# Performance work log

Measured on AMD Instinct MI355X. Metric: run time of the kernel, lower is better.

The kernel has to match this reference:

```python
import jax, jax.numpy as jnp
import numpy as np

FS = 11        # filter_size
N_ITER = 5     # mean-field iterations


def _unfold(x, fs):
    """x: (B, C, Hp, Wp) padded -> patches (B, C, H, W, fs, fs) with
    patches[b,c,h,w,i,j] == x[b,c,h+i,w+j]."""
    B, C, Hp, Wp = x.shape
    H, W = Hp - fs + 1, Wp - fs + 1
    p = jax.lax.conv_general_dilated_patches(
        x.reshape(B * C, 1, Hp, Wp), (fs, fs), (1, 1), 'VALID')  # (B*C, fs*fs, H, W)
    return p.reshape(B, C, fs, fs, H, W).transpose(0, 1, 4, 5, 2, 3)


def _smoothing_filter(fs, inv_bw, spacings):
    """Gaussian spatial filter with zeroed center, shape (B, fs, fs)."""
    r = jnp.arange(-(fs // 2), fs // 2 + 1, dtype=spacings.dtype)
    d = jnp.stack(jnp.meshgrid(r, r, indexing='ij'))           # (2, fs, fs)
    d = d[None] * spacings[:, :, None, None]                   # (B, 2, fs, fs)
    f = jnp.exp(-jnp.sum((d * inv_bw) ** 2 / 2, axis=1))       # (B, fs, fs)
    return f.at[:, fs // 2, fs // 2].set(0.0)


def setup_inputs() -> dict:
    key = jax.random.key(0)
    k1, k2 = jax.random.split(key)
    B, C, CH, H, W = 2, 6, 3, 192, 192
    return {
        'x': jax.random.normal(k1, (B, C, H, W), dtype=jnp.float32),
        'features': jax.random.normal(k2, (B, CH, H, W), dtype=jnp.float32),
        'spatial_spacings': jnp.ones((B, 2), dtype=jnp.float32),
        'smoothing_weight': jnp.array(1.0, dtype=jnp.float32),
        'appearance_weight': jnp.array(1.0, dtype=jnp.float32),
        'inverse_smoothing_bandwidth': jnp.array(1.0, dtype=jnp.float32),
        'inverse_appearance_bandwidth': jnp.array(1.0, dtype=jnp.float32),
    }


def reference(x, features, spatial_spacings, smoothing_weight, appearance_weight,
              inverse_smoothing_bandwidth, inverse_appearance_bandwidth):
    fs, pad = FS, FS // 2
    B, C, H, W = x.shape
    pad_cfg = [(0, 0), (0, 0), (pad, pad), (pad, pad)]

    # Spatial Gaussian filter (iteration-independent).
    sf = _smoothing_filter(fs, inverse_smoothing_bandwidth, spatial_spacings)  # (B,fs,fs)

    # Bilateral (appearance) filter, also iteration-independent -> hoisted.
    fpatch = _unfold(jnp.pad(features, pad_cfg), fs)           # (B,ch,H,W,fs,fs)
    diffs = features[..., None, None] - fpatch
    af = jnp.exp(-jnp.sum((diffs * inverse_appearance_bandwidth) ** 2 / 2, axis=1))  # (B,H,W,fs,fs)
    af = af.at[..., fs // 2, fs // 2].set(0.0)

    # combined message filter: w_s * sf + w_a * sf * af  (center tap already zero)
    sfb = sf[:, None, None]                                    # (B,1,1,fs,fs)
    total_filter = smoothing_weight * jnp.broadcast_to(sfb, af.shape) + appearance_weight * sfb * af

    compat = -jnp.eye(C, dtype=x.dtype)                        # Potts compatibility mu(l,l') = -[l==l']
    negative_unary = x
    for _ in range(N_ITER):
        q = jax.nn.softmax(x, axis=1)
        qpatch = _unfold(jnp.pad(q, pad_cfg), fs)              # (B,C,H,W,fs,fs)
        msg = jnp.einsum('bhwij,bchwij->bchw', total_filter, qpatch)
        x = negative_unary - jnp.einsum('bjhw,jk->bkhw', msg, compat)
    return jax.nn.log_softmax(x, axis=1)
```

## Files before the change

### kernel.cpp

```cpp
#include <hip/hip_runtime.h>

#define HH 192
#define WW 192
#define BB 2
#define NC 6
#define FSZ 11
#define PAD 5
#define TW 16
#define TH 8
#define SWD 26
#define SHT 18
#define LA 27
#define HW (HH*WW)
#define NWV 12
#define BT (NWV*64)
#define NPX (TW*TH)

__device__ __forceinline__ unsigned pkbf(float a, float b) {
    unsigned ua = (__float_as_uint(a) + 0x8000u) >> 16;
    unsigned ub = (__float_as_uint(b) + 0x8000u) & 0xffff0000u;
    return ua | ub;
}
__device__ __forceinline__ float lo16(unsigned u){ return __uint_as_float(u << 16); }
__device__ __forceinline__ float hi16(unsigned u){ return __uint_as_float(u & 0xffff0000u); }

template<bool FIRST, bool LAST>
__global__ __launch_bounds__(BT, 6)
void crf_it(const float* __restrict__ xpl, const uint4* __restrict__ Ain,
            const float* __restrict__ f2in, const float* __restrict__ feats,
            const float* __restrict__ spac, const float* __restrict__ swp,
            const float* __restrict__ awp, const float* __restrict__ isbp,
            const float* __restrict__ iabp,
            uint4* __restrict__ Aout, float* __restrict__ f2out,
            float* __restrict__ outp)
{
    __shared__ uint4 A[SHT][LA];
    __shared__ float F2[SHT][LA];
    __shared__ float sfw[FSZ*FSZ];
    __shared__ float sfa[FSZ*FSZ];
    __shared__ float pm[NWV][NC][132];

    const int tid = threadIdx.x;
    const int b  = blockIdx.z;
    const int w0 = blockIdx.x * TW;
    const int h0 = blockIdx.y * TH;

    const float sw  = swp[0], aw = awp[0], isb = isbp[0], iab = iabp[0];
    const float s0  = spac[b*2], s1 = spac[b*2+1];
    const float sfac = iab * 0.70710678f;

    if (tid < FSZ*FSZ) {
        const int fi = tid / FSZ, fj = tid - (tid/FSZ)*FSZ;
        const float ri = (float)(fi-PAD) * s0 * isb;
        const float rj = (float)(fj-PAD) * s1 * isb;
        float sf = __expf(-0.5f*(ri*ri + rj*rj));
        if (fi == PAD && fj == PAD) sf = 0.f;
        sfw[tid] = sf * sw;
        sfa[tid] = sf * aw;
    }

    if (tid < SHT*SWD) {
        const int sr = tid / SWD, sc = tid - (tid/SWD)*SWD;
        const int gh = h0 + sr - PAD, gw = w0 + sc - PAD;
        uint4 av = make_uint4(0u,0u,0u,0u);
        float f2v = 0.f;
        if (gh >= 0 && gh < HH && gw >= 0 && gw < WW) {
            if (FIRST) {
                const int off = gh*WW + gw;
                const float* xb = xpl + (size_t)b*NC*HW + off;
                const float v0 = xb[0], v1 = xb[HW], v2 = xb[2*HW];
                const float v3 = xb[3*HW], v4 = xb[4*HW], v5 = xb[5*HW];
                float m = fmaxf(fmaxf(fmaxf(v0,v1),fmaxf(v2,v3)),fmaxf(v4,v5));
                float q0=__expf(v0-m), q1=__expf(v1-m), q2=__expf(v2-m);
                float q3=__expf(v3-m), q4=__expf(v4-m), q5=__expf(v5-m);
                const float rs = 1.0f/(q0+q1+q2+q3+q4+q5);
                const float* fb = feats + (size_t)b*3*HW + off;
                const float g0 = fb[0]*sfac, g1 = fb[HW]*sfac;
                f2v = fb[2*HW]*sfac;
                av = make_uint4(pkbf(q0*rs,q1*rs), pkbf(q2*rs,q3*rs),
                                pkbf(q4*rs,q5*rs), pkbf(g0,g1));
            } else {
                const size_t p = (size_t)(b*HH + gh)*WW + gw;
                av  = Ain[p];
                f2v = f2in[p];
            }
        }
        A[sr][sc]  = av;
        F2[sr][sc] = f2v;
    }
    __syncthreads();

    const int w    = tid >> 6;
    const int l    = tid & 63;
    const int half = l >> 5;
    const int lh   = l & 31;
    const int ry   = lh >> 2;
    const int c0   = (lh & 3) * 4;

    int row, jbase, jcnt;
    if (w == 5)       { row = 5; jbase = half ? 6 : 0; jcnt = 3; }
    else if (w == 11) { row = 5; jbase = half ? 9 : 3; jcnt = half ? 2 : 3; }
    else              { row = w; jbase = half ? 6 : 0; jcnt = half ? 5 : 6; }
    const int asteps = jcnt + 3;

    float srwR[6], sraR[6];
    #pragma unroll
    for (int d = 0; d < 6; ++d) {
        const int j = jbase + d;
        const bool v = (d < jcnt) && (j < FSZ);
        srwR[d] = v ? sfw[row*FSZ + j] : 0.f;
        sraR[d] = v ? sfa[row*FSZ + j] : 0.f;
    }

    float cf0[4], cf1[4], cf2[4];
    #pragma unroll
    for (int k = 0; k < 4; ++k) {
        const unsigned fw = A[ry+PAD][c0+PAD+k].w;
        cf0[k] = lo16(fw);
        cf1[k] = hi16(fw);
        cf2[k] = F2[ry+PAD][c0+PAD+k];
    }

    float2 m01[4], m23[4], m45[4];
    #pragma unroll
    for (int k = 0; k < 4; ++k) {
        m01[k]=make_float2(0.f,0.f); m23[k]=make_float2(0.f,0.f); m45[k]=make_float2(0.f,0.f);
    }

    const uint4* Ar = &A[ry + row][c0 + jbase];
    const float* Fr = &F2[ry + row][c0 + jbase];
    #pragma unroll
    for (int a = 0; a < 9; ++a) {
        if (a < asteps) {
            const uint4 av = Ar[a];
            const float g2 = Fr[a];
            const float q0 = lo16(av.x), q1 = hi16(av.x);
            const float q2 = lo16(av.y), q3 = hi16(av.y);
            const float q4 = lo16(av.z), q5 = hi16(av.z);
            const float g0 = lo16(av.w), g1 = hi16(av.w);
            #pragma unroll
            for (int k = 0; k < 4; ++k) {
                const int d = a - k;
                if (0 <= d && d < 6) {
                    const float d0 = cf0[k]-g0, d1 = cf1[k]-g1, d2 = cf2[k]-g2;
                    const float t  = fmaf(d2,d2, fmaf(d1,d1, d0*d0));
                    const float af = __expf(-t);
                    const float tf = fmaf(af, sraR[d], srwR[d]);
                    m01[k].x = fmaf(tf,q0,m01[k].x); m01[k].y = fmaf(tf,q1,m01[k].y);
                    m23[k].x = fmaf(tf,q2,m23[k].x); m23[k].y = fmaf(tf,q3,m23[k].y);
                    m45[k].x = fmaf(tf,q4,m45[k].x); m45[k].y = fmaf(tf,q5,m45[k].y);
                }
            }
        }
    }

    #pragma unroll
    for (int k = 0; k < 4; ++k) {
        m01[k].x += __shfl_xor(m01[k].x, 32); m01[k].y += __shfl_xor(m01[k].y, 32);
        m23[k].x += __shfl_xor(m23[k].x, 32); m23[k].y += __shfl_xor(m23[k].y, 32);
        m45[k].x += __shfl_xor(m45[k].x, 32); m45[k].y += __shfl_xor(m45[k].y, 32);
    }

    if (half == 0) {
        const int px = ry*16 + c0;
        *(float4*)&pm[w][0][px] = make_float4(m01[0].x, m01[1].x, m01[2].x, m01[3].x);
        *(float4*)&pm[w][1][px] = make_float4(m01[0].y, m01[1].y, m01[2].y, m01[3].y);
        *(float4*)&pm[w][2][px] = make_float4(m23[0].x, m23[1].x, m23[2].x, m23[3].x);
        *(float4*)&pm[w][3][px] = make_float4(m23[0].y, m23[1].y, m23[2].y, m23[3].y);
        *(float4*)&pm[w][4][px] = make_float4(m45[0].x, m45[1].x, m45[2].x, m45[3].x);
        *(float4*)&pm[w][5][px] = make_float4(m45[0].y, m45[1].y, m45[2].y, m45[3].y);
    }
    __syncthreads();

    if (tid < NPX) {
        const int pr = tid >> 4, pc = tid & 15;
        const int oh = h0 + pr, ow = w0 + pc;
        const size_t pb = (size_t)b*NC*HW + (size_t)oh*WW + ow;
        float xn[NC];
        #pragma unroll
        for (int c = 0; c < NC; ++c) {
            float s = 0.f;
            #pragma unroll
            for (int g = 0; g < NWV; ++g) s += pm[g][c][tid];
            xn[c] = s + xpl[pb + (size_t)c*HW];
        }

        float m = xn[0];
        #pragma unroll
        for (int c = 1; c < NC; ++c) m = fmaxf(m, xn[c]);

        if (LAST) {
            float s = 0.f;
            #pragma unroll
            for (int c = 0; c < NC; ++c) s += __expf(xn[c]-m);
            const float lg = m + __logf(s);
            #pragma unroll
            for (int c = 0; c < NC; ++c) outp[pb + (size_t)c*HW] = xn[c] - lg;
        } else {
            float e[NC], s = 0.f;
            #pragma unroll
            for (int c = 0; c < NC; ++c) { e[c] = __expf(xn[c]-m); s += e[c]; }
            const float rs = 1.0f / s;
            const int r5 = pr + PAD, c5 = pc + PAD;
            const size_t p = (size_t)(b*HH + oh)*WW + ow;
            Aout[p] = make_uint4(pkbf(e[0]*rs,e[1]*rs), pkbf(e[2]*rs,e[3]*rs),
                                 pkbf(e[4]*rs,e[5]*rs), A[r5][c5].w);
            if (FIRST) f2out[p] = F2[r5][c5];
        }
    }
}

extern "C" void kernel_launch(void* const* d_in, const int* in_sizes, int n_in,
                              void* d_out, int out_size, void* d_ws, size_t ws_size,
                              hipStream_t stream)
{
    const float* x    = (const float*)d_in[0];
    const float* fts  = (const float*)d_in[1];
    const float* spc  = (const float*)d_in[2];
    const float* swp  = (const float*)d_in[3];
    const float* awp  = (const float*)d_in[4];
    const float* isbp = (const float*)d_in[5];
    const float* iabp = (const float*)d_in[6];
    float* out = (float*)d_out;

    uint4* A0  = (uint4*)d_ws;
    uint4* A1  = A0 + (size_t)BB*HW;
    float* f2s = (float*)(A1 + (size_t)BB*HW);

    dim3 grid(WW/TW, HH/TH, BB);
    dim3 blk(BT);

    crf_it<true ,false><<<grid, blk, 0, stream>>>(x, A1, f2s, fts, spc, swp, awp, isbp, iabp, A0, f2s, out);
    crf_it<false,false><<<grid, blk, 0, stream>>>(x, A0, f2s, fts, spc, swp, awp, isbp, iabp, A1, f2s, out);
    crf_it<false,false><<<grid, blk, 0, stream>>>(x, A1, f2s, fts, spc, swp, awp, isbp, iabp, A0, f2s, out);
    crf_it<false,false><<<grid, blk, 0, stream>>>(x, A0, f2s, fts, spc, swp, awp, isbp, iabp, A1, f2s, out);
    crf_it<false,true ><<<grid, blk, 0, stream>>>(x, A1, f2s, fts, spc, swp, awp, isbp, iabp, A0, f2s, out);
}
```

Before: 63.01 us.

## Retile CRF iteration to 96x3 tiles with shuffle-only tap reduction

Changes the tile from 16x8 to 96x3 pixels per block, so the halo overhead is smaller relative to the tile. Each group of 8 lanes now handles 3 adjacent pixels and splits the 11x11 taps across lanes. The partial sums are combined with xor shuffles, which replaces the shared-memory partial-message buffer and the second barrier. The trade-off is a higher register count per thread (18 accumulators) and fewer blocks per CU (launch bounds drop from 6 to 3). The halo load is now a strided loop.

```diff
diff --git a/kernel.cpp b/kernel.cpp
--- a/kernel.cpp
+++ b/kernel.cpp
@@ -6,15 +6,13 @@
 #define NC 6
 #define FSZ 11
 #define PAD 5
-#define TW 16
-#define TH 8
-#define SWD 26
-#define SHT 18
-#define LA 27
+#define TW 96
+#define TH 3
+#define SWD 107
+#define SHT 14
+#define LA 107
 #define HW (HH*WW)
-#define NWV 12
-#define BT (NWV*64)
-#define NPX (TW*TH)
+#define BT 768
 
 __device__ __forceinline__ unsigned pkbf(float a, float b) {
     unsigned ua = (__float_as_uint(a) + 0x8000u) >> 16;
@@ -25,7 +23,7 @@
 __device__ __forceinline__ float hi16(unsigned u){ return __uint_as_float(u & 0xffff0000u); }
 
 template<bool FIRST, bool LAST>
-__global__ __launch_bounds__(BT, 6)
+__global__ __launch_bounds__(BT, 3)
 void crf_it(const float* __restrict__ xpl, const uint4* __restrict__ Ain,
             const float* __restrict__ f2in, const float* __restrict__ feats,
             const float* __restrict__ spac, const float* __restrict__ swp,
@@ -38,7 +36,6 @@
     __shared__ float F2[SHT][LA];
     __shared__ float sfw[FSZ*FSZ];
     __shared__ float sfa[FSZ*FSZ];
-    __shared__ float pm[NWV][NC][132];
 
     const int tid = threadIdx.x;
     const int b  = blockIdx.z;
@@ -59,8 +56,8 @@
         sfa[tid] = sf * aw;
     }
 
-    if (tid < SHT*SWD) {
-        const int sr = tid / SWD, sc = tid - (tid/SWD)*SWD;
+    for (int idx = tid; idx < SHT*SWD; idx += BT) {
+        const int sr = idx / SWD, sc = idx - (idx/SWD)*SWD;
         const int gh = h0 + sr - PAD, gw = w0 + sc - PAD;
         uint4 av = make_uint4(0u,0u,0u,0u);
         float f2v = 0.f;
@@ -92,46 +89,44 @@
 
     const int w    = tid >> 6;
     const int l    = tid & 63;
-    const int half = l >> 5;
-    const int lh   = l & 31;
-    const int ry   = lh >> 2;
-    const int c0   = (lh & 3) * 4;
-
-    int row, jbase, jcnt;
-    if (w == 5)       { row = 5; jbase = half ? 6 : 0; jcnt = 3; }
-    else if (w == 11) { row = 5; jbase = half ? 9 : 3; jcnt = half ? 2 : 3; }
-    else              { row = w; jbase = half ? 6 : 0; jcnt = half ? 5 : 6; }
-    const int asteps = jcnt + 3;
-
-    float srwR[6], sraR[6];
-    #pragma unroll
-    for (int d = 0; d < 6; ++d) {
-        const int j = jbase + d;
-        const bool v = (d < jcnt) && (j < FSZ);
-        srwR[d] = v ? sfw[row*FSZ + j] : 0.f;
-        sraR[d] = v ? sfa[row*FSZ + j] : 0.f;
-    }
-
-    float cf0[4], cf1[4], cf2[4];
-    #pragma unroll
-    for (int k = 0; k < 4; ++k) {
-        const unsigned fw = A[ry+PAD][c0+PAD+k].w;
-        cf0[k] = lo16(fw);
-        cf1[k] = hi16(fw);
-        cf2[k] = F2[ry+PAD][c0+PAD+k];
-    }
-
-    float2 m01[4], m23[4], m45[4];
-    #pragma unroll
-    for (int k = 0; k < 4; ++k) {
-        m01[k]=make_float2(0.f,0.f); m23[k]=make_float2(0.f,0.f); m45[k]=make_float2(0.f,0.f);
-    }
-
-    const uint4* Ar = &A[ry + row][c0 + jbase];
-    const float* Fr = &F2[ry + row][c0 + jbase];
-    #pragma unroll
-    for (int a = 0; a < 9; ++a) {
-        if (a < asteps) {
+    const int t3   = l >> 3;
+    const int rb   = (l >> 1) & 3;
+    const int hf   = l & 1;
+    const int prow = w >> 2;
+    const int cb   = (w & 3)*24 + t3*3;
+    const int jb   = hf*6;
+    const int jcnt = hf ? 5 : 6;
+
+    float cf0[3], cf1[3], cf2[3];
+    #pragma unroll
+    for (int k = 0; k < 3; ++k) {
+        const uint4 cav = A[prow+PAD][cb+k+PAD];
+        cf0[k] = lo16(cav.w);
+        cf1[k] = hi16(cav.w);
+        cf2[k] = F2[prow+PAD][cb+k+PAD];
+    }
+
+    float ms[3][NC];
+    #pragma unroll
+    for (int k = 0; k < 3; ++k)
+        #pragma unroll
+        for (int c = 0; c < NC; ++c) ms[k][c] = 0.f;
+
+    #pragma unroll
+    for (int m = 0; m < 3; ++m) {
+        const int i = rb + 4*m;
+        const bool vrow = (i < FSZ);
+        float srwR[6], sraR[6];
+        #pragma unroll
+        for (int d = 0; d < 6; ++d) {
+            const bool v = vrow && (d < jcnt);
+            srwR[d] = v ? sfw[i*FSZ + jb + d] : 0.f;
+            sraR[d] = v ? sfa[i*FSZ + jb + d] : 0.f;
+        }
+        const uint4* Ar = &A[prow + i][cb + jb];
+        const float* Fr = &F2[prow + i][cb + jb];
+        #pragma unroll
+        for (int a = 0; a < 8; ++a) {
             const uint4 av = Ar[a];
             const float g2 = Fr[a];
             const float q0 = lo16(av.x), q1 = hi16(av.x);
@@ -139,73 +134,65 @@
             const float q4 = lo16(av.z), q5 = hi16(av.z);
             const float g0 = lo16(av.w), g1 = hi16(av.w);
             #pragma unroll
-            for (int k = 0; k < 4; ++k) {
+            for (int k = 0; k < 3; ++k) {
                 const int d = a - k;
                 if (0 <= d && d < 6) {
                     const float d0 = cf0[k]-g0, d1 = cf1[k]-g1, d2 = cf2[k]-g2;
                     const float t  = fmaf(d2,d2, fmaf(d1,d1, d0*d0));
                     const float af = __expf(-t);
                     const float tf = fmaf(af, sraR[d], srwR[d]);
-                    m01[k].x = fmaf(tf,q0,m01[k].x); m01[k].y = fmaf(tf,q1,m01[k].y);
-                    m23[k].x = fmaf(tf,q2,m23[k].x); m23[k].y = fmaf(tf,q3,m23[k].y);
-                    m45[k].x = fmaf(tf,q4,m45[k].x); m45[k].y = fmaf(tf,q5,m45[k].y);
+                    ms[k][0] = fmaf(tf,q0,ms[k][0]);
+                    ms[k][1] = fmaf(tf,q1,ms[k][1]);
+                    ms[k][2] = fmaf(tf,q2,ms[k][2]);
+                    ms[k][3] = fmaf(tf,q3,ms[k][3]);
+                    ms[k][4] = fmaf(tf,q4,ms[k][4]);
+                    ms[k][5] = fmaf(tf,q5,ms[k][5]);
                 }
             }
         }
     }
 
     #pragma unroll
-    for (int k = 0; k < 4; ++k) {
-        m01[k].x += __shfl_xor(m01[k].x, 32); m01[k].y += __shfl_xor(m01[k].y, 32);
-        m23[k].x += __shfl_xor(m23[k].x, 32); m23[k].y += __shfl_xor(m23[k].y, 32);
-        m45[k].x += __shfl_xor(m45[k].x, 32); m45[k].y += __shfl_xor(m45[k].y, 32);
-    }
-
-    if (half == 0) {
-        const int px = ry*16 + c0;
-        *(float4*)&pm[w][0][px] = make_float4(m01[0].x, m01[1].x, m01[2].x, m01[3].x);
-        *(float4*)&pm[w][1][px] = make_float4(m01[0].y, m01[1].y, m01[2].y, m01[3].y);
-        *(float4*)&pm[w][2][px] = make_float4(m23[0].x, m23[1].x, m23[2].x, m23[3].x);
-        *(float4*)&pm[w][3][px] = make_float4(m23[0].y, m23[1].y, m23[2].y, m23[3].y);
-        *(float4*)&pm[w][4][px] = make_float4(m45[0].x, m45[1].x, m45[2].x, m45[3].x);
-        *(float4*)&pm[w][5][px] = make_float4(m45[0].y, m45[1].y, m45[2].y, m45[3].y);
-    }
-    __syncthreads();
-
-    if (tid < NPX) {
-        const int pr = tid >> 4, pc = tid & 15;
-        const int oh = h0 + pr, ow = w0 + pc;
-        const size_t pb = (size_t)b*NC*HW + (size_t)oh*WW + ow;
-        float xn[NC];
+    for (int k = 0; k < 3; ++k)
         #pragma unroll
         for (int c = 0; c < NC; ++c) {
-            float s = 0.f;
+            float v = ms[k][c];
+            v += __shfl_xor(v, 1);
+            v += __shfl_xor(v, 2);
+            v += __shfl_xor(v, 4);
+            ms[k][c] = v;
+        }
+
+    if ((l & 7) == 0) {
+        #pragma unroll
+        for (int k = 0; k < 3; ++k) {
+            const int oh = h0 + prow, ow = w0 + cb + k;
+            const size_t pb = (size_t)b*NC*HW + (size_t)oh*WW + ow;
+            float xn[NC];
             #pragma unroll
-            for (int g = 0; g < NWV; ++g) s += pm[g][c][tid];
-            xn[c] = s + xpl[pb + (size_t)c*HW];
-        }
-
-        float m = xn[0];
-        #pragma unroll
-        for (int c = 1; c < NC; ++c) m = fmaxf(m, xn[c]);
-
-        if (LAST) {
-            float s = 0.f;
+            for (int c = 0; c < NC; ++c) xn[c] = ms[k][c] + xpl[pb + (size_t)c*HW];
+
+            float m = xn[0];
             #pragma unroll
-            for (int c = 0; c < NC; ++c) s += __expf(xn[c]-m);
-            const float lg = m + __logf(s);
-            #pragma unroll
-            for (int c = 0; c < NC; ++c) outp[pb + (size_t)c*HW] = xn[c] - lg;
-        } else {
-            float e[NC], s = 0.f;
-            #pragma unroll
-            for (int c = 0; c < NC; ++c) { e[c] = __expf(xn[c]-m); s += e[c]; }
-            const float rs = 1.0f / s;
-            const int r5 = pr + PAD, c5 = pc + PAD;
-            const size_t p = (size_t)(b*HH + oh)*WW + ow;
-            Aout[p] = make_uint4(pkbf(e[0]*rs,e[1]*rs), pkbf(e[2]*rs,e[3]*rs),
-                                 pkbf(e[4]*rs,e[5]*rs), A[r5][c5].w);
-            if (FIRST) f2out[p] = F2[r5][c5];
+            for (int c = 1; c < NC; ++c) m = fmaxf(m, xn[c]);
+
+            if (LAST) {
+                float s = 0.f;
+                #pragma unroll
+                for (int c = 0; c < NC; ++c) s += __expf(xn[c]-m);
+                const float lg = m + __logf(s);
+                #pragma unroll
+                for (int c = 0; c < NC; ++c) outp[pb + (size_t)c*HW] = xn[c] - lg;
+            } else {
+                float e[NC], s = 0.f;
+                #pragma unroll
+                for (int c = 0; c < NC; ++c) { e[c] = __expf(xn[c]-m); s += e[c]; }
+                const float rs = 1.0f / s;
+                const size_t p = (size_t)(b*HH + oh)*WW + ow;
+                Aout[p] = make_uint4(pkbf(e[0]*rs,e[1]*rs), pkbf(e[2]*rs,e[3]*rs),
+                                     pkbf(e[4]*rs,e[5]*rs), pkbf(cf0[k],cf1[k]));
+                if (FIRST) f2out[p] = cf2[k];
+            }
         }
     }
 }
```

New measurement: 65.69 us. 4.3% more time.
